# Kernel tuning notes

Hardware: AMD Instinct MI355X
Metric: run time of the kernel (lower is better)

Reference implementation:

```python
import jax, jax.numpy as jnp
import numpy as np

N_NODES = 50000
N_EDGES = 800000
D_NODE = 128
D_EDGE = 16
HID = 64
EPS = 1e-5


def _sage_conv(x, src, dst, Wl, bl, Wr, n_nodes):
    # PyG SAGEConv (mean aggr): out = lin_l(mean_{src->dst} x[src]) + lin_r(x)
    msg = x[src]                                        # [E, F] gather
    s = jax.ops.segment_sum(msg, dst, num_segments=n_nodes)   # [N, F]
    cnt = jax.ops.segment_sum(jnp.ones((src.shape[0],), x.dtype), dst,
                              num_segments=n_nodes)
    agg = s / jnp.maximum(cnt, 1.0)[:, None]
    return agg @ Wl.T + bl + x @ Wr.T


def _batchnorm(h, gamma, beta):
    # training-mode BN over node dim (biased variance, as in torch)
    mu = jnp.mean(h, axis=0)
    var = jnp.mean((h - mu) ** 2, axis=0)
    return gamma * (h - mu) / jnp.sqrt(var + EPS) + beta


def setup_inputs() -> dict:
    key = jax.random.key(0)
    ks = jax.random.split(key, 16)
    def lin(k, out_f, in_f):
        lim = 1.0 / np.sqrt(in_f)
        return jax.random.uniform(k, (out_f, in_f), jnp.float32, -lim, lim)
    x = jax.random.normal(ks[0], (N_NODES, D_NODE), jnp.float32)
    edge_index = jax.random.randint(ks[1], (2, N_EDGES), 0, N_NODES, jnp.int64)
    edge_attr = jax.random.normal(ks[2], (N_EDGES, D_EDGE), jnp.float32)
    return {
        "x": x, "edge_index": edge_index, "edge_attr": edge_attr,
        # SAGEConv 1
        "W1l": lin(ks[3], HID, D_NODE), "b1l": jnp.zeros((HID,), jnp.float32),
        "W1r": lin(ks[4], HID, D_NODE),
        "g1": jnp.ones((HID,), jnp.float32), "be1": jnp.zeros((HID,), jnp.float32),
        # SAGEConv 2
        "W2l": lin(ks[5], HID, HID), "b2l": jnp.zeros((HID,), jnp.float32),
        "W2r": lin(ks[6], HID, HID),
        "g2": jnp.ones((HID,), jnp.float32), "be2": jnp.zeros((HID,), jnp.float32),
        # edge MLP: (2*HID + D_EDGE) -> 128 -> 64 -> 2
        "Wm1": lin(ks[7], 128, 2 * HID + D_EDGE), "bm1": jnp.zeros((128,), jnp.float32),
        "Wm2": lin(ks[8], 64, 128), "bm2": jnp.zeros((64,), jnp.float32),
        "Wm3": lin(ks[9], 2, 64), "bm3": jnp.zeros((2,), jnp.float32),
    }


def reference(x, edge_index, edge_attr,
              W1l, b1l, W1r, g1, be1,
              W2l, b2l, W2r, g2, be2,
              Wm1, bm1, Wm2, bm2, Wm3, bm3):
    src, dst = edge_index[0], edge_index[1]
    n = x.shape[0]
    h = _sage_conv(x, src, dst, W1l, b1l, W1r, n)
    h = jax.nn.relu(_batchnorm(h, g1, be1))          # dropout = identity (eval)
    h = _sage_conv(h, src, dst, W2l, b2l, W2r, n)
    h = jax.nn.relu(_batchnorm(h, g2, be2))
    edge_in = jnp.concatenate([h[src], edge_attr, h[dst]], axis=1)  # [E, 144]
    z = jax.nn.relu(edge_in @ Wm1.T + bm1)
    z = jax.nn.relu(z @ Wm2.T + bm2)
    return z @ Wm3.T + bm3                           # [E, 2] logits
```

## Files before the change

### kernel.cpp

```cpp
#include <hip/hip_runtime.h>
#include <hip/hip_fp16.h>


#define EPS 1e-5f

typedef _Float16 h8 __attribute__((ext_vector_type(8)));
typedef float f32x4 __attribute__((ext_vector_type(4)));

__global__ __launch_bounds__(256) void k_prep_hist(
    const float* __restrict__ W1l, const float* __restrict__ W1r,
    const float* __restrict__ b1l,
    const float* __restrict__ W2l, const float* __restrict__ W2r,
    const float* __restrict__ b2l,
    const float* __restrict__ Wm1, const float* __restrict__ Wm2,
    float* __restrict__ Wt1, float* __restrict__ Wt2,
    float* __restrict__ bias1, float* __restrict__ bias2,
    __half* __restrict__ W2B, __half* __restrict__ W1B,
    const int* __restrict__ dst, int* __restrict__ deg, int E, int prepBlocks) {
  if ((int)blockIdx.x >= prepBlocks) {
    int e = (blockIdx.x - prepBlocks) * 256 + threadIdx.x;
    if (e < E) atomicAdd(&deg[dst[e]], 1);
    return;
  }
  int idx = blockIdx.x * 256 + threadIdx.x;
  if (idx < 16384) {
    int k = idx >> 7, f = idx & 127;
    Wt1[idx] = (f < 64) ? W1l[f * 128 + k] : W1r[(f - 64) * 128 + k];
    return;
  }
  idx -= 16384;
  if (idx < 8192) {
    int k = idx >> 7, f = idx & 127;
    Wt2[idx] = (f < 64) ? W2l[f * 64 + k] : W2r[(f - 64) * 64 + k];
    return;
  }
  idx -= 8192;
  if (idx < 128) { bias1[idx] = (idx < 64) ? 0.f : b1l[idx - 64]; return; }
  idx -= 128;
  if (idx < 128) { bias2[idx] = (idx < 64) ? 0.f : b2l[idx - 64]; return; }
  idx -= 128;
  if (idx < 8192) {
    int j = idx & 7, l = (idx >> 3) & 63, f = idx >> 9;
    int kc = f >> 2, tt = f & 3;
    int col = 16 * tt + (l & 15);
    int k = 32 * kc + (l >> 4) * 8 + j;
    W2B[idx] = __float2half(Wm2[col * 128 + k]);
    return;
  }
  idx -= 8192;
  if (idx < 20480) {
    int j = idx & 7, l = (idx >> 3) & 63, f = idx >> 9;
    int kc = f >> 3, nc = f & 7;
    int k = 32 * kc + (l >> 4) * 8 + j;
    int n = 16 * nc + (l & 15);
    float w;
    if (k < 64)       w = Wm1[n * 144 + k];
    else if (k < 128) w = Wm1[n * 144 + 80 + (k - 64)];
    else if (k < 144) w = Wm1[n * 144 + 64 + (k - 128)];
    else              w = 0.f;
    W1B[idx] = __float2half(w);
    return;
  }
}

__global__ __launch_bounds__(1024) void k_scan(
    const int* __restrict__ deg, int* __restrict__ rowptr,
    int* __restrict__ cursor, int N) {
  __shared__ int wsum[16];
  __shared__ int carry;
  const int lane = threadIdx.x & 63;
  const int w    = threadIdx.x >> 6;
  if (threadIdx.x == 0) carry = 0;
  __syncthreads();
  for (int base = 0; base < N; base += 1024) {
    int i = base + threadIdx.x;
    int v = (i < N) ? deg[i] : 0;
    int incl = v;
#pragma unroll
    for (int off = 1; off < 64; off <<= 1) {
      int t = __shfl_up(incl, off);
      if (lane >= off) incl += t;
    }
    if (lane == 63) wsum[w] = incl;
    __syncthreads();
    if (w == 0) {
      int ws_ = (lane < 16) ? wsum[lane] : 0;
      int wincl = ws_;
#pragma unroll
      for (int off = 1; off < 16; off <<= 1) {
        int t = __shfl_up(wincl, off);
        if (lane >= off) wincl += t;
      }
      if (lane < 16) wsum[lane] = wincl;
    }
    __syncthreads();
    int woff = carry + (w > 0 ? wsum[w - 1] : 0);
    int excl = woff + incl - v;
    if (i < N) { rowptr[i] = excl; cursor[i] = excl; }
    int tot = wsum[15];
    __syncthreads();
    if (threadIdx.x == 0) carry += tot;
    __syncthreads();
  }
  if (threadIdx.x == 0) rowptr[N] = carry;
}

__global__ __launch_bounds__(256) void k_fill(
    const int* __restrict__ src, const int* __restrict__ dst,
    const float* __restrict__ attr,
    int* __restrict__ cursor, int2* __restrict__ csr_sd,
    int* __restrict__ pos, __half* __restrict__ attrC, int E) {
  int e = blockIdx.x * 256 + threadIdx.x;
  if (e < E) {
    int d = dst[e];
    int p = atomicAdd(&cursor[d], 1);
    csr_sd[p] = make_int2(src[e], d);
    pos[e] = p;
    const float4* at4 = (const float4*)attr;
    float4 a0 = at4[(size_t)e * 4 + 0];
    float4 a1 = at4[(size_t)e * 4 + 1];
    float4 a2 = at4[(size_t)e * 4 + 2];
    float4 a3 = at4[(size_t)e * 4 + 3];
    __half2 hh[8];
    hh[0] = __floats2half2_rn(a0.x, a0.y);
    hh[1] = __floats2half2_rn(a0.z, a0.w);
    hh[2] = __floats2half2_rn(a1.x, a1.y);
    hh[3] = __floats2half2_rn(a1.z, a1.w);
    hh[4] = __floats2half2_rn(a2.x, a2.y);
    hh[5] = __floats2half2_rn(a2.z, a2.w);
    hh[6] = __floats2half2_rn(a3.x, a3.y);
    hh[7] = __floats2half2_rn(a3.z, a3.w);
    *(uint4*)&attrC[(size_t)p * 16]     = *(uint4*)&hh[0];
    *(uint4*)&attrC[(size_t)p * 16 + 8] = *(uint4*)&hh[4];
  }
}

__global__ __launch_bounds__(256) void k_scatter_out(
    const float* __restrict__ out2, const int* __restrict__ pos,
    float* __restrict__ out, int E) {
  int e = blockIdx.x * 256 + threadIdx.x;
  if (e < E) {
    int p = pos[e];
    *(float2*)&out[(size_t)e * 2] = *(const float2*)&out2[(size_t)p * 2];
  }
}

template<int K, int MODE>
__global__ __launch_bounds__(256) void k_gemm(
    const float* __restrict__ X, const float* __restrict__ stats,
    const float* __restrict__ gma, const float* __restrict__ bta,
    const float* __restrict__ Wt, const float* __restrict__ bias,
    __half* __restrict__ outH, float* __restrict__ outF, int N, int Ftot) {
  __shared__ __align__(16) float Xs[32][68];
  __shared__ __align__(16) float Ws_[32][128];
  __shared__ float scs[64], shs[64];
  const int tid = threadIdx.x;
  const int tx  = tid & 15;
  const int ty  = tid >> 4;
  const int n0  = blockIdx.x * 64;
  if (stats && tid < 64) {
    float s0 = 0.f, s1 = 0.f;
#pragma unroll
    for (int r = 0; r < 8; ++r) {
      s0 += stats[r * 128 + tid];
      s1 += stats[r * 128 + 64 + tid];
    }
    float inv_n = 1.0f / (float)N;
    float mean = s0 * inv_n;
    float var  = s1 * inv_n - mean * mean;
    float s = gma[tid] * rsqrtf(var + EPS);
    scs[tid] = s;
    shs[tid] = bta[tid] - mean * s;
  }
  float acc[4][8];
#pragma unroll
  for (int j = 0; j < 8; ++j) {
    float bv = bias[8 * tx + j];
#pragma unroll
    for (int i = 0; i < 4; ++i) acc[i][j] = bv;
  }
  for (int k0 = 0; k0 < K; k0 += 32) {
    __syncthreads();
#pragma unroll
    for (int l = 0; l < 2; ++l) {
      int idx = tid * 2 + l;
      int kq = idx & 7, n = idx >> 3;
      float4 xv = make_float4(0.f, 0.f, 0.f, 0.f);
      if (n0 + n < N) xv = *(const float4*)&X[(size_t)(n0 + n) * K + k0 + kq * 4];
      if (stats) {
        int kb = k0 + kq * 4;
        xv.x = fmaxf(xv.x * scs[kb + 0] + shs[kb + 0], 0.f);
        xv.y = fmaxf(xv.y * scs[kb + 1] + shs[kb + 1], 0.f);
        xv.z = fmaxf(xv.z * scs[kb + 2] + shs[kb + 2], 0.f);
        xv.w = fmaxf(xv.w * scs[kb + 3] + shs[kb + 3], 0.f);
      }
      Xs[kq * 4 + 0][n] = xv.x;
      Xs[kq * 4 + 1][n] = xv.y;
      Xs[kq * 4 + 2][n] = xv.z;
      Xs[kq * 4 + 3][n] = xv.w;
    }
#pragma unroll
    for (int l = 0; l < 4; ++l) {
      int idx = tid + l * 256;
      int kr = idx >> 5, fc = idx & 31;
      *(float4*)&Ws_[kr][fc * 4] =
          *(const float4*)&Wt[(size_t)(k0 + kr) * Ftot + fc * 4];
    }
    __syncthreads();
#pragma unroll
    for (int kk = 0; kk < 32; ++kk) {
      float4 a  = *(const float4*)&Xs[kk][4 * ty];
      float4 b0 = *(const float4*)&Ws_[kk][8 * tx];
      float4 b1 = *(const float4*)&Ws_[kk][8 * tx + 4];
      float aa[4] = {a.x, a.y, a.z, a.w};
      float bb[8] = {b0.x, b0.y, b0.z, b0.w, b1.x, b1.y, b1.z, b1.w};
#pragma unroll
      for (int i = 0; i < 4; ++i)
#pragma unroll
        for (int j = 0; j < 8; ++j) acc[i][j] += aa[i] * bb[j];
    }
  }
#pragma unroll
  for (int i = 0; i < 4; ++i) {
    int n = n0 + 4 * ty + i;
    if (n >= N) continue;
    if (tx < 8) {
      __half2 hh[4];
#pragma unroll
      for (int c = 0; c < 4; ++c)
        hh[c] = __floats2half2_rn(acc[i][2 * c], acc[i][2 * c + 1]);
      *(uint4*)&outH[(size_t)n * 64 + 8 * tx] = *(uint4*)hh;
    } else {
      float* cp = outF + (size_t)n * 64 + 8 * tx - 64;
      *(float4*)cp = make_float4(acc[i][0], acc[i][1], acc[i][2], acc[i][3]);
      *(float4*)(cp + 4) = make_float4(acc[i][4], acc[i][5], acc[i][6], acc[i][7]);
    }
  }
}

__global__ __launch_bounds__(256) void k_agg(
    const __half* __restrict__ qb, const float* __restrict__ pb,
    const int* __restrict__ rowptr, const int2* __restrict__ csr_sd,
    float* __restrict__ hpre, float* __restrict__ stats, int N) {
  __shared__ float red[512];
  const int tid  = threadIdx.x;
  const int w    = tid >> 6;
  const int lane = tid & 63;
  const int g    = lane >> 3, c = lane & 7;
  float lsum = 0.f, lsq = 0.f;
  const int wid = blockIdx.x * 4 + w;
  const int nw  = gridDim.x * 4;
  for (int n = wid; n < N; n += nw) {
    const int r0 = rowptr[n], r1 = rowptr[n + 1];
    float s[8] = {0.f, 0.f, 0.f, 0.f, 0.f, 0.f, 0.f, 0.f};
    for (int j = r0 + g; j < r1; j += 8) {
      int a = csr_sd[j].x;
      uint4 rv = *(const uint4*)&qb[(size_t)a * 64 + 8 * c];
      const __half2* hp = (const __half2*)&rv;
#pragma unroll
      for (int q = 0; q < 4; ++q) {
        float2 f2 = __half22float2(hp[q]);
        s[2 * q]     += f2.x;
        s[2 * q + 1] += f2.y;
      }
    }
#pragma unroll
    for (int m = 8; m < 64; m <<= 1)
#pragma unroll
      for (int q = 0; q < 8; ++q) s[q] += __shfl_xor(s[q], m);
    float sv = s[0];
#pragma unroll
    for (int q = 1; q < 8; ++q) sv = (g == q) ? s[q] : sv;
    float cdeg = (float)(r1 - r0);
    cdeg = cdeg > 1.f ? cdeg : 1.f;
    const int f = 8 * c + g;
    float v = sv / cdeg + pb[(size_t)n * 64 + f];
    hpre[(size_t)n * 64 + f] = v;
    lsum += v;
    lsq  += v * v;
  }
  red[tid]       = lsum;
  red[256 + tid] = lsq;
  __syncthreads();
  if (tid < 64) {
    float ts = red[tid] + red[tid + 64] + red[tid + 128] + red[tid + 192];
    float tq = red[256 + tid] + red[256 + tid + 64] + red[256 + tid + 128] + red[256 + tid + 192];
    int f = 8 * (tid & 7) + (tid >> 3);
    float* st = stats + (blockIdx.x & 7) * 128;
    atomicAdd(&st[f], ts);
    atomicAdd(&st[64 + f], tq);
  }
}

__global__ __launch_bounds__(256) void k_bn(
    const float* __restrict__ H1, const float* __restrict__ stats,
    const float* __restrict__ g, const float* __restrict__ be,
    __half* __restrict__ H2, int N) {
  __shared__ float scs[64], shs[64];
  const int tid = threadIdx.x;
  if (tid < 64) {
    float s0 = 0.f, s1 = 0.f;
#pragma unroll
    for (int r = 0; r < 8; ++r) {
      s0 += stats[r * 128 + tid];
      s1 += stats[r * 128 + 64 + tid];
    }
    float inv_n = 1.0f / (float)N;
    float mean = s0 * inv_n;
    float var  = s1 * inv_n - mean * mean;
    float s = g[tid] * rsqrtf(var + EPS);
    scs[tid] = s;
    shs[tid] = be[tid] - mean * s;
  }
  __syncthreads();
  int idx = blockIdx.x * 256 + tid;
  if (idx >= N * 8) return;
  int n = idx >> 3, f8 = (idx & 7) * 8;
  float4 h0 = *(const float4*)&H1[(size_t)n * 64 + f8];
  float4 h1 = *(const float4*)&H1[(size_t)n * 64 + f8 + 4];
  __half2 hh[4];
  hh[0] = __floats2half2_rn(fmaxf(h0.x * scs[f8 + 0] + shs[f8 + 0], 0.f),
                            fmaxf(h0.y * scs[f8 + 1] + shs[f8 + 1], 0.f));
  hh[1] = __floats2half2_rn(fmaxf(h0.z * scs[f8 + 2] + shs[f8 + 2], 0.f),
                            fmaxf(h0.w * scs[f8 + 3] + shs[f8 + 3], 0.f));
  hh[2] = __floats2half2_rn(fmaxf(h1.x * scs[f8 + 4] + shs[f8 + 4], 0.f),
                            fmaxf(h1.y * scs[f8 + 5] + shs[f8 + 5], 0.f));
  hh[3] = __floats2half2_rn(fmaxf(h1.z * scs[f8 + 6] + shs[f8 + 6], 0.f),
                            fmaxf(h1.w * scs[f8 + 7] + shs[f8 + 7], 0.f));
  *(uint4*)&H2[(size_t)n * 64 + f8] = *(uint4*)hh;
}

__global__ __launch_bounds__(256, 2) void k_edge(
    const __half* __restrict__ H2, const __half* __restrict__ attrC,
    const int2* __restrict__ csd,
    const __half* __restrict__ W1Bws, const __half* __restrict__ W2Bws,
    const float* __restrict__ bm1, const float* __restrict__ bm2,
    const float* __restrict__ Wm3, const float* __restrict__ bm3,
    float* __restrict__ out2, int E) {
  __shared__ __align__(16) _Float16 W1B[20480];
  __shared__ __align__(16) _Float16 W2B[8192];
  __shared__ __align__(16) _Float16 Z1f[64 * 136];

  const int tid  = threadIdx.x;
  const int lane = tid & 63;
  const int w    = tid >> 6;
  const int ln15 = lane & 15;
  const int quad = lane >> 4;

  for (int i = tid; i < 2560; i += 256)
    ((uint4*)W1B)[i] = ((const uint4*)W1Bws)[i];
  for (int i = tid; i < 1024; i += 256)
    ((uint4*)W2B)[i] = ((const uint4*)W2Bws)[i];

  float bm1v[8];
#pragma unroll
  for (int nc = 0; nc < 8; ++nc) bm1v[nc] = bm1[16 * nc + ln15];
  float bmv[4], w30[4], w31[4];
#pragma unroll
  for (int t = 0; t < 4; ++t) {
    bmv[t] = bm2[16 * t + ln15];
    w30[t] = Wm3[16 * t + ln15];
    w31[t] = Wm3[64 + 16 * t + ln15];
  }
  const float bm30 = bm3[0], bm31 = bm3[1];
  __syncthreads();

  const int nt = (E + 63) >> 6;
  const int rowoff = 16 * w + ln15;

  for (int t = blockIdx.x; t < nt; t += gridDim.x) {
    int er = (t << 6) + rowoff;
    if (er >= E) er = E - 1;
    const int2 sd = csd[er];
    const int s = sd.x;
    const int d = sd.y;

    h8 af0 = *(const h8*)&H2[(size_t)s * 64 + 8 * quad];
    h8 af1 = *(const h8*)&H2[(size_t)s * 64 + 32 + 8 * quad];
    h8 af2 = *(const h8*)&H2[(size_t)d * 64 + 8 * quad];
    h8 af3 = *(const h8*)&H2[(size_t)d * 64 + 32 + 8 * quad];
    h8 af4 = (h8){0, 0, 0, 0, 0, 0, 0, 0};
    if (quad < 2)
      af4 = *(const h8*)&attrC[(size_t)er * 16 + 8 * quad];

    const int ebase = 16 * w + 4 * quad;
#pragma unroll
    for (int nc = 0; nc < 8; ++nc) {
      f32x4 a1 = (f32x4){bm1v[nc], bm1v[nc], bm1v[nc], bm1v[nc]};
      a1 = __builtin_amdgcn_mfma_f32_16x16x32_f16(
          af0, *(const h8*)&W1B[((0 * 8 + nc) << 9) + (lane << 3)], a1, 0, 0, 0);
      a1 = __builtin_amdgcn_mfma_f32_16x16x32_f16(
          af1, *(const h8*)&W1B[((1 * 8 + nc) << 9) + (lane << 3)], a1, 0, 0, 0);
      a1 = __builtin_amdgcn_mfma_f32_16x16x32_f16(
          af2, *(const h8*)&W1B[((2 * 8 + nc) << 9) + (lane << 3)], a1, 0, 0, 0);
      a1 = __builtin_amdgcn_mfma_f32_16x16x32_f16(
          af3, *(const h8*)&W1B[((3 * 8 + nc) << 9) + (lane << 3)], a1, 0, 0, 0);
      a1 = __builtin_amdgcn_mfma_f32_16x16x32_f16(
          af4, *(const h8*)&W1B[((4 * 8 + nc) << 9) + (lane << 3)], a1, 0, 0, 0);
      Z1f[(ebase + 0) * 136 + 16 * nc + ln15] = (_Float16)fmaxf(a1[0], 0.f);
      Z1f[(ebase + 1) * 136 + 16 * nc + ln15] = (_Float16)fmaxf(a1[1], 0.f);
      Z1f[(ebase + 2) * 136 + 16 * nc + ln15] = (_Float16)fmaxf(a1[2], 0.f);
      Z1f[(ebase + 3) * 136 + 16 * nc + ln15] = (_Float16)fmaxf(a1[3], 0.f);
    }

    f32x4 acc2[4];
#pragma unroll
    for (int tt = 0; tt < 4; ++tt)
      acc2[tt] = (f32x4){bmv[tt], bmv[tt], bmv[tt], bmv[tt]};
#pragma unroll
    for (int kc = 0; kc < 4; ++kc) {
      h8 a = *(const h8*)&Z1f[(16 * w + ln15) * 136 + 32 * kc + 8 * quad];
#pragma unroll
      for (int tt = 0; tt < 4; ++tt) {
        h8 bf = *(const h8*)&W2B[((kc * 4 + tt) * 64 + lane) * 8];
        acc2[tt] = __builtin_amdgcn_mfma_f32_16x16x32_f16(a, bf, acc2[tt], 0, 0, 0);
      }
    }

    float p0[4], p1[4];
#pragma unroll
    for (int r = 0; r < 4; ++r) { p0[r] = 0.f; p1[r] = 0.f; }
#pragma unroll
    for (int tt = 0; tt < 4; ++tt)
#pragma unroll
      for (int r = 0; r < 4; ++r) {
        float z = fmaxf(acc2[tt][r], 0.f);
        p0[r] += z * w30[tt];
        p1[r] += z * w31[tt];
      }
#pragma unroll
    for (int r = 0; r < 4; ++r) {
#pragma unroll
      for (int m = 1; m < 16; m <<= 1) {
        p0[r] += __shfl_xor(p0[r], m);
        p1[r] += __shfl_xor(p1[r], m);
      }
      if (ln15 == 0) {
        int j = (t << 6) + 16 * w + 4 * quad + r;
        if (j < E)
          *(float2*)&out2[(size_t)j * 2] = make_float2(p0[r] + bm30, p1[r] + bm31);
      }
    }
  }
}

extern "C" void kernel_launch(void* const* d_in, const int* in_sizes, int n_in,
                              void* d_out, int out_size, void* d_ws, size_t ws_size,
                              hipStream_t stream) {
  const float* x    = (const float*)d_in[0];
  const int*   ei   = (const int*)d_in[1];
  const float* attr = (const float*)d_in[2];
  const float* W1l  = (const float*)d_in[3];
  const float* b1l  = (const float*)d_in[4];
  const float* W1r  = (const float*)d_in[5];
  const float* g1   = (const float*)d_in[6];
  const float* be1  = (const float*)d_in[7];
  const float* W2l  = (const float*)d_in[8];
  const float* b2l  = (const float*)d_in[9];
  const float* W2r  = (const float*)d_in[10];
  const float* g2   = (const float*)d_in[11];
  const float* be2  = (const float*)d_in[12];
  const float* Wm1  = (const float*)d_in[13];
  const float* bm1  = (const float*)d_in[14];
  const float* Wm2  = (const float*)d_in[15];
  const float* bm2  = (const float*)d_in[16];
  const float* Wm3  = (const float*)d_in[17];
  const float* bm3  = (const float*)d_in[18];
  float* out = (float*)d_out;

  const int N = in_sizes[0] / 128;
  const int E = in_sizes[1] / 2;
  const int* srcI = ei;
  const int* dstI = ei + E;

  float* ws = (float*)d_ws;
  const size_t NF = (size_t)N * 64;
  float*  P32 = ws;
  float*  H1  = ws + NF;
  __half* Q16 = (__half*)(ws + 2 * NF);
  float* small  = ws + 2 * NF + NF / 2;
  float* stats1 = small;
  float* stats2 = stats1 + 1024;
  float* Wt1    = stats2 + 1024;
  float* Wt2    = Wt1 + 16384;
  float* bias1  = Wt2 + 8192;
  float* bias2  = bias1 + 128;
  __half* W1B   = (__half*)(bias2 + 128);
  __half* W2B   = (__half*)(bias2 + 128 + 10240);
  int2* csr_sd = (int2*)(bias2 + 128 + 10240 + 4096);
  int* rowptr = (int*)(csr_sd + E);
  int* cursor = rowptr + (N + 1);
  int* deg    = cursor + N;
  int* pos    = deg + N;
  __half* attrC = (__half*)(((uintptr_t)(pos + E) + 15) & ~(uintptr_t)15);

  __half* H2  = Q16;
  float* out2 = H1;

  hipMemsetAsync(deg, 0, (size_t)N * sizeof(int), stream);
  hipMemsetAsync(stats1, 0, 2048 * sizeof(float), stream);

  const int eBlocks = (E + 255) / 256;
  const int prepBlocks = (53504 + 255) / 256;
  k_prep_hist<<<prepBlocks + eBlocks, 256, 0, stream>>>(
      W1l, W1r, b1l, W2l, W2r, b2l, Wm1, Wm2,
      Wt1, Wt2, bias1, bias2, W2B, W1B,
      dstI, deg, E, prepBlocks);
  k_scan<<<1, 1024, 0, stream>>>(deg, rowptr, cursor, N);
  k_fill<<<eBlocks, 256, 0, stream>>>(srcI, dstI, attr, cursor,
                                      csr_sd, pos, attrC, E);

  const int mTiles = (N + 63) / 64;

  k_gemm<128, 0><<<mTiles, 256, 0, stream>>>(x, nullptr, nullptr, nullptr,
                                             Wt1, bias1, Q16, P32, N, 128);
  k_agg<<<1024, 256, 0, stream>>>(Q16, P32, rowptr, csr_sd, H1, stats1, N);

  k_gemm<64, 0><<<mTiles, 256, 0, stream>>>(H1, stats1, g1, be1,
                                            Wt2, bias2, Q16, P32, N, 128);
  k_agg<<<1024, 256, 0, stream>>>(Q16, P32, rowptr, csr_sd, H1, stats2, N);

  k_bn<<<(N * 8 + 255) / 256, 256, 0, stream>>>(H1, stats2, g2, be2, H2, N);

  k_edge<<<1024, 256, 0, stream>>>(H2, attrC, csr_sd,
                                   W1B, W2B, bm1, bm2, Wm3, bm3, out2, E);
  k_scatter_out<<<eBlocks, 256, 0, stream>>>(out2, pos, out, E);
}
```

Measured before the change: 492.9 us.

## Process two edge subtiles per wave in edge MLP, read W2 from global

The edge MLP kernel now handles 128 edges per block iteration: each wave computes two 16-row MFMA tiles that share every W1 and W2 fragment load, and the Z1 staging buffer doubles in size. The shared-memory copy of W2 is dropped and its fragments are read straight from global memory through cache, trading LDS for global traffic. Separately, the BN statistics atomics are spread over 32 partial slots instead of 8 to reduce atomic contention, which means the stats memset and the reduction loops grow accordingly. More accumulators and fragments per wave raise register pressure, which can hurt occupancy under the 2-blocks-per-SM launch bound.

```diff
diff --git a/kernel.cpp b/kernel.cpp
--- a/kernel.cpp
+++ b/kernel.cpp
@@ -161,7 +161,7 @@
   if (stats && tid < 64) {
     float s0 = 0.f, s1 = 0.f;
 #pragma unroll
-    for (int r = 0; r < 8; ++r) {
+    for (int r = 0; r < 32; ++r) {
       s0 += stats[r * 128 + tid];
       s1 += stats[r * 128 + 64 + tid];
     }
@@ -286,7 +286,7 @@
     float ts = red[tid] + red[tid + 64] + red[tid + 128] + red[tid + 192];
     float tq = red[256 + tid] + red[256 + tid + 64] + red[256 + tid + 128] + red[256 + tid + 192];
     int f = 8 * (tid & 7) + (tid >> 3);
-    float* st = stats + (blockIdx.x & 7) * 128;
+    float* st = stats + (blockIdx.x & 31) * 128;
     atomicAdd(&st[f], ts);
     atomicAdd(&st[64 + f], tq);
   }
@@ -301,7 +301,7 @@
   if (tid < 64) {
     float s0 = 0.f, s1 = 0.f;
 #pragma unroll
-    for (int r = 0; r < 8; ++r) {
+    for (int r = 0; r < 32; ++r) {
       s0 += stats[r * 128 + tid];
       s1 += stats[r * 128 + 64 + tid];
     }
@@ -338,8 +338,7 @@
     const float* __restrict__ Wm3, const float* __restrict__ bm3,
     float* __restrict__ out2, int E) {
   __shared__ __align__(16) _Float16 W1B[20480];
-  __shared__ __align__(16) _Float16 W2B[8192];
-  __shared__ __align__(16) _Float16 Z1f[64 * 136];
+  __shared__ __align__(16) _Float16 Z1f[128 * 136];
 
   const int tid  = threadIdx.x;
   const int lane = tid & 63;
@@ -349,8 +348,6 @@
 
   for (int i = tid; i < 2560; i += 256)
     ((uint4*)W1B)[i] = ((const uint4*)W1Bws)[i];
-  for (int i = tid; i < 1024; i += 256)
-    ((uint4*)W2B)[i] = ((const uint4*)W2Bws)[i];
 
   float bm1v[8];
 #pragma unroll
@@ -365,80 +362,132 @@
   const float bm30 = bm3[0], bm31 = bm3[1];
   __syncthreads();
 
-  const int nt = (E + 63) >> 6;
-  const int rowoff = 16 * w + ln15;
+  const int nt = (E + 127) >> 7;
+  const int rowA = 32 * w + ln15;
+  const int rowB = 32 * w + 16 + ln15;
 
   for (int t = blockIdx.x; t < nt; t += gridDim.x) {
-    int er = (t << 6) + rowoff;
-    if (er >= E) er = E - 1;
-    const int2 sd = csd[er];
-    const int s = sd.x;
-    const int d = sd.y;
-
-    h8 af0 = *(const h8*)&H2[(size_t)s * 64 + 8 * quad];
-    h8 af1 = *(const h8*)&H2[(size_t)s * 64 + 32 + 8 * quad];
-    h8 af2 = *(const h8*)&H2[(size_t)d * 64 + 8 * quad];
-    h8 af3 = *(const h8*)&H2[(size_t)d * 64 + 32 + 8 * quad];
-    h8 af4 = (h8){0, 0, 0, 0, 0, 0, 0, 0};
-    if (quad < 2)
-      af4 = *(const h8*)&attrC[(size_t)er * 16 + 8 * quad];
-
-    const int ebase = 16 * w + 4 * quad;
+    const int e0 = t << 7;
+    int erA = e0 + rowA; if (erA >= E) erA = E - 1;
+    int erB = e0 + rowB; if (erB >= E) erB = E - 1;
+    const int2 sdA = csd[erA];
+    const int2 sdB = csd[erB];
+
+    h8 aA0 = *(const h8*)&H2[(size_t)sdA.x * 64 + 8 * quad];
+    h8 aA1 = *(const h8*)&H2[(size_t)sdA.x * 64 + 32 + 8 * quad];
+    h8 aA2 = *(const h8*)&H2[(size_t)sdA.y * 64 + 8 * quad];
+    h8 aA3 = *(const h8*)&H2[(size_t)sdA.y * 64 + 32 + 8 * quad];
+    h8 aB0 = *(const h8*)&H2[(size_t)sdB.x * 64 + 8 * quad];
+    h8 aB1 = *(const h8*)&H2[(size_t)sdB.x * 64 + 32 + 8 * quad];
+    h8 aB2 = *(const h8*)&H2[(size_t)sdB.y * 64 + 8 * quad];
+    h8 aB3 = *(const h8*)&H2[(size_t)sdB.y * 64 + 32 + 8 * quad];
+    h8 aA4 = (h8){0, 0, 0, 0, 0, 0, 0, 0};
+    h8 aB4 = (h8){0, 0, 0, 0, 0, 0, 0, 0};
+    if (quad < 2) {
+      aA4 = *(const h8*)&attrC[(size_t)erA * 16 + 8 * quad];
+      aB4 = *(const h8*)&attrC[(size_t)erB * 16 + 8 * quad];
+    }
+
+    const int ebA = 32 * w + 4 * quad;
+    const int ebB = 32 * w + 16 + 4 * quad;
 #pragma unroll
     for (int nc = 0; nc < 8; ++nc) {
-      f32x4 a1 = (f32x4){bm1v[nc], bm1v[nc], bm1v[nc], bm1v[nc]};
-      a1 = __builtin_amdgcn_mfma_f32_16x16x32_f16(
-          af0, *(const h8*)&W1B[((0 * 8 + nc) << 9) + (lane << 3)], a1, 0, 0, 0);
-      a1 = __builtin_amdgcn_mfma_f32_16x16x32_f16(
-          af1, *(const h8*)&W1B[((1 * 8 + nc) << 9) + (lane << 3)], a1, 0, 0, 0);
-      a1 = __builtin_amdgcn_mfma_f32_16x16x32_f16(
-          af2, *(const h8*)&W1B[((2 * 8 + nc) << 9) + (lane << 3)], a1, 0, 0, 0);
-      a1 = __builtin_amdgcn_mfma_f32_16x16x32_f16(
-          af3, *(const h8*)&W1B[((3 * 8 + nc) << 9) + (lane << 3)], a1, 0, 0, 0);
-      a1 = __builtin_amdgcn_mfma_f32_16x16x32_f16(
-          af4, *(const h8*)&W1B[((4 * 8 + nc) << 9) + (lane << 3)], a1, 0, 0, 0);
-      Z1f[(ebase + 0) * 136 + 16 * nc + ln15] = (_Float16)fmaxf(a1[0], 0.f);
-      Z1f[(ebase + 1) * 136 + 16 * nc + ln15] = (_Float16)fmaxf(a1[1], 0.f);
-      Z1f[(ebase + 2) * 136 + 16 * nc + ln15] = (_Float16)fmaxf(a1[2], 0.f);
-      Z1f[(ebase + 3) * 136 + 16 * nc + ln15] = (_Float16)fmaxf(a1[3], 0.f);
-    }
-
-    f32x4 acc2[4];
-#pragma unroll
-    for (int tt = 0; tt < 4; ++tt)
-      acc2[tt] = (f32x4){bmv[tt], bmv[tt], bmv[tt], bmv[tt]};
+      f32x4 cA = (f32x4){bm1v[nc], bm1v[nc], bm1v[nc], bm1v[nc]};
+      f32x4 cB = cA;
+      h8 bf;
+      bf = *(const h8*)&W1B[((0 * 8 + nc) << 9) + (lane << 3)];
+      cA = __builtin_amdgcn_mfma_f32_16x16x32_f16(aA0, bf, cA, 0, 0, 0);
+      cB = __builtin_amdgcn_mfma_f32_16x16x32_f16(aB0, bf, cB, 0, 0, 0);
+      bf = *(const h8*)&W1B[((1 * 8 + nc) << 9) + (lane << 3)];
+      cA = __builtin_amdgcn_mfma_f32_16x16x32_f16(aA1, bf, cA, 0, 0, 0);
+      cB = __builtin_amdgcn_mfma_f32_16x16x32_f16(aB1, bf, cB, 0, 0, 0);
+      bf = *(const h8*)&W1B[((2 * 8 + nc) << 9) + (lane << 3)];
+      cA = __builtin_amdgcn_mfma_f32_16x16x32_f16(aA2, bf, cA, 0, 0, 0);
+      cB = __builtin_amdgcn_mfma_f32_16x16x32_f16(aB2, bf, cB, 0, 0, 0);
+      bf = *(const h8*)&W1B[((3 * 8 + nc) << 9) + (lane << 3)];
+      cA = __builtin_amdgcn_mfma_f32_16x16x32_f16(aA3, bf, cA, 0, 0, 0);
+      cB = __builtin_amdgcn_mfma_f32_16x16x32_f16(aB3, bf, cB, 0, 0, 0);
+      bf = *(const h8*)&W1B[((4 * 8 + nc) << 9) + (lane << 3)];
+      cA = __builtin_amdgcn_mfma_f32_16x16x32_f16(aA4, bf, cA, 0, 0, 0);
+      cB = __builtin_amdgcn_mfma_f32_16x16x32_f16(aB4, bf, cB, 0, 0, 0);
+      Z1f[(ebA + 0) * 136 + 16 * nc + ln15] = (_Float16)fmaxf(cA[0], 0.f);
+      Z1f[(ebA + 1) * 136 + 16 * nc + ln15] = (_Float16)fmaxf(cA[1], 0.f);
+      Z1f[(ebA + 2) * 136 + 16 * nc + ln15] = (_Float16)fmaxf(cA[2], 0.f);
+      Z1f[(ebA + 3) * 136 + 16 * nc + ln15] = (_Float16)fmaxf(cA[3], 0.f);
+      Z1f[(ebB + 0) * 136 + 16 * nc + ln15] = (_Float16)fmaxf(cB[0], 0.f);
+      Z1f[(ebB + 1) * 136 + 16 * nc + ln15] = (_Float16)fmaxf(cB[1], 0.f);
+      Z1f[(ebB + 2) * 136 + 16 * nc + ln15] = (_Float16)fmaxf(cB[2], 0.f);
+      Z1f[(ebB + 3) * 136 + 16 * nc + ln15] = (_Float16)fmaxf(cB[3], 0.f);
+    }
+
+    f32x4 c2A[4], c2B[4];
+#pragma unroll
+    for (int tt = 0; tt < 4; ++tt) {
+      c2A[tt] = (f32x4){bmv[tt], bmv[tt], bmv[tt], bmv[tt]};
+      c2B[tt] = c2A[tt];
+    }
 #pragma unroll
     for (int kc = 0; kc < 4; ++kc) {
-      h8 a = *(const h8*)&Z1f[(16 * w + ln15) * 136 + 32 * kc + 8 * quad];
+      h8 zA = *(const h8*)&Z1f[(32 * w + ln15) * 136 + 32 * kc + 8 * quad];
+      h8 zB = *(const h8*)&Z1f[(32 * w + 16 + ln15) * 136 + 32 * kc + 8 * quad];
 #pragma unroll
       for (int tt = 0; tt < 4; ++tt) {
-        h8 bf = *(const h8*)&W2B[((kc * 4 + tt) * 64 + lane) * 8];
-        acc2[tt] = __builtin_amdgcn_mfma_f32_16x16x32_f16(a, bf, acc2[tt], 0, 0, 0);
+        h8 bf = *(const h8*)&W2Bws[((kc * 4 + tt) * 64 + lane) * 8];
+        c2A[tt] = __builtin_amdgcn_mfma_f32_16x16x32_f16(zA, bf, c2A[tt], 0, 0, 0);
+        c2B[tt] = __builtin_amdgcn_mfma_f32_16x16x32_f16(zB, bf, c2B[tt], 0, 0, 0);
       }
     }
 
-    float p0[4], p1[4];
-#pragma unroll
-    for (int r = 0; r < 4; ++r) { p0[r] = 0.f; p1[r] = 0.f; }
-#pragma unroll
-    for (int tt = 0; tt < 4; ++tt)
+    {
+      float p0[4], p1[4];
+#pragma unroll
+      for (int r = 0; r < 4; ++r) { p0[r] = 0.f; p1[r] = 0.f; }
+#pragma unroll
+      for (int tt = 0; tt < 4; ++tt)
+#pragma unroll
+        for (int r = 0; r < 4; ++r) {
+          float z = fmaxf(c2A[tt][r], 0.f);
+          p0[r] += z * w30[tt];
+          p1[r] += z * w31[tt];
+        }
 #pragma unroll
       for (int r = 0; r < 4; ++r) {
-        float z = fmaxf(acc2[tt][r], 0.f);
-        p0[r] += z * w30[tt];
-        p1[r] += z * w31[tt];
+#pragma unroll
+        for (int m = 1; m < 16; m <<= 1) {
+          p0[r] += __shfl_xor(p0[r], m);
+          p1[r] += __shfl_xor(p1[r], m);
+        }
+        if (ln15 == 0) {
+          int j = e0 + 32 * w + 4 * quad + r;
+          if (j < E)
+            *(float2*)&out2[(size_t)j * 2] = make_float2(p0[r] + bm30, p1[r] + bm31);
+        }
       }
-#pragma unroll
-    for (int r = 0; r < 4; ++r) {
-#pragma unroll
-      for (int m = 1; m < 16; m <<= 1) {
-        p0[r] += __shfl_xor(p0[r], m);
-        p1[r] += __shfl_xor(p1[r], m);
-      }
-      if (ln15 == 0) {
-        int j = (t << 6) + 16 * w + 4 * quad + r;
-        if (j < E)
-          *(float2*)&out2[(size_t)j * 2] = make_float2(p0[r] + bm30, p1[r] + bm31);
+    }
+    {
+      float p0[4], p1[4];
+#pragma unroll
+      for (int r = 0; r < 4; ++r) { p0[r] = 0.f; p1[r] = 0.f; }
+#pragma unroll
+      for (int tt = 0; tt < 4; ++tt)
+#pragma unroll
+        for (int r = 0; r < 4; ++r) {
+          float z = fmaxf(c2B[tt][r], 0.f);
+          p0[r] += z * w30[tt];
+          p1[r] += z * w31[tt];
+        }
+#pragma unroll
+      for (int r = 0; r < 4; ++r) {
+#pragma unroll
+        for (int m = 1; m < 16; m <<= 1) {
+          p0[r] += __shfl_xor(p0[r], m);
+          p1[r] += __shfl_xor(p1[r], m);
+        }
+        if (ln15 == 0) {
+          int j = e0 + 32 * w + 16 + 4 * quad + r;
+          if (j < E)
+            *(float2*)&out2[(size_t)j * 2] = make_float2(p0[r] + bm30, p1[r] + bm31);
+        }
       }
     }
   }
@@ -480,8 +529,8 @@
   __half* Q16 = (__half*)(ws + 2 * NF);
   float* small  = ws + 2 * NF + NF / 2;
   float* stats1 = small;
-  float* stats2 = stats1 + 1024;
-  float* Wt1    = stats2 + 1024;
+  float* stats2 = stats1 + 4096;
+  float* Wt1    = stats2 + 4096;
   float* Wt2    = Wt1 + 16384;
   float* bias1  = Wt2 + 8192;
   float* bias2  = bias1 + 128;
@@ -498,7 +547,7 @@
   float* out2 = H1;
 
   hipMemsetAsync(deg, 0, (size_t)N * sizeof(int), stream);
-  hipMemsetAsync(stats1, 0, 2048 * sizeof(float), stream);
+  hipMemsetAsync(stats1, 0, 8192 * sizeof(float), stream);
 
   const int eBlocks = (E + 255) / 256;
   const int prepBlocks = (53504 + 255) / 256;
```

Measured after the change: 484.7 us. About the same (-1.7%).
